# Performance work log

Hardware: AMD Instinct MI355X
Metric: run time of the kernel (lower is better)

Reference implementation:

```python
import jax, jax.numpy as jnp
import numpy as np

N_NODES = 50000
N_EDGES = 800000
IN_CH = 128
HID = 256


def gcn_layer(x, src, dst, W, b, n_nodes):
    # x: [N, F_in] -> h: [N, F_out]
    h = x @ W
    # add self loops (PyG GCNConv default)
    loop = jnp.arange(n_nodes, dtype=src.dtype)
    src_f = jnp.concatenate([src, loop])
    dst_f = jnp.concatenate([dst, loop])
    # symmetric normalization: deg^{-1/2}[src] * deg^{-1/2}[dst]
    deg = jax.ops.segment_sum(jnp.ones_like(dst_f, dtype=h.dtype), dst_f, num_segments=n_nodes)
    dinv = jnp.where(deg > 0, jax.lax.rsqrt(deg), 0.0)
    norm = dinv[src_f] * dinv[dst_f]  # [E+N]
    msg = h[src_f] * norm[:, None]    # [E+N, F_out] gather
    out = jax.ops.segment_sum(msg, dst_f, num_segments=n_nodes)  # scatter-add
    return out + b


def setup_inputs() -> dict:
    key = jax.random.key(0)
    k1, k2, k3, k4 = jax.random.split(key, 4)
    x = jax.random.normal(k1, (N_NODES, IN_CH), dtype=jnp.float32)
    edge_index = jax.random.randint(k2, (2, N_EDGES), 0, N_NODES, dtype=jnp.int64)
    W1 = jax.random.normal(k3, (IN_CH, HID), dtype=jnp.float32) * (1.0 / np.sqrt(IN_CH))
    b1 = jnp.zeros((HID,), dtype=jnp.float32)
    W2 = jax.random.normal(k4, (HID, HID), dtype=jnp.float32) * (1.0 / np.sqrt(HID))
    b2 = jnp.zeros((HID,), dtype=jnp.float32)
    return {"x": x, "edge_index": edge_index, "W1": W1, "b1": b1, "W2": W2, "b2": b2}


def reference(x, edge_index, W1, b1, W2, b2):
    src, dst = edge_index[0], edge_index[1]
    h = gcn_layer(x, src, dst, W1, b1, N_NODES)
    h = jax.nn.relu(h)
    # dropout in eval mode (training=False) is identity
    out = gcn_layer(h, src, dst, W2, b2, N_NODES)
    return out
```

## Files before the change

kernel.cpp:

```cpp
#include <hip/hip_runtime.h>

constexpr int N = 50000;
constexpr int E = 800000;
constexpr int NPAD = 50048;
constexpr int NB = (N + 255) / 256;

typedef _Float16 half8 __attribute__((ext_vector_type(8)));
typedef _Float16 half4v __attribute__((ext_vector_type(4)));
typedef float float4v __attribute__((ext_vector_type(4)));

__global__ __launch_bounds__(256) void deg_kernel(const int* __restrict__ dst,
                                                  int* __restrict__ degI) {
    int e = blockIdx.x * 256 + threadIdx.x;
    if (e < E) atomicAdd(&degI[dst[e]], 1);
}

__global__ __launch_bounds__(256) void dinv_kernel(const int* __restrict__ degI,
                                                   float* __restrict__ dinv) {
    int v = blockIdx.x * 256 + threadIdx.x;
    if (v < N) dinv[v] = rsqrtf((float)degI[v] + 1.0f);
}

__global__ __launch_bounds__(256) void scan1_kernel(const int* __restrict__ degI,
                                                    int* __restrict__ incl,
                                                    int* __restrict__ blockSums) {
    __shared__ int s[256];
    int t = threadIdx.x;
    int i = blockIdx.x * 256 + t;
    int d = (i < N) ? degI[i] : 0;
    s[t] = d;
    __syncthreads();
    for (int off = 1; off < 256; off <<= 1) {
        int v = s[t];
        int u = (t >= off) ? s[t - off] : 0;
        __syncthreads();
        s[t] = v + u;
        __syncthreads();
    }
    if (i < N) incl[i] = s[t];
    if (t == 255) blockSums[blockIdx.x] = s[255];
}

__global__ __launch_bounds__(256) void scan2_kernel(int* __restrict__ blockSums) {
    __shared__ int s[256];
    int t = threadIdx.x;
    int v = (t < NB) ? blockSums[t] : 0;
    s[t] = v;
    __syncthreads();
    for (int off = 1; off < 256; off <<= 1) {
        int a = s[t];
        int u = (t >= off) ? s[t - off] : 0;
        __syncthreads();
        s[t] = a + u;
        __syncthreads();
    }
    if (t < NB) blockSums[t] = s[t] - v;
}

__global__ __launch_bounds__(256) void scan3_kernel(const int* __restrict__ degI,
                                                    const int* __restrict__ incl,
                                                    const int* __restrict__ blockSums,
                                                    int* __restrict__ rowptr,
                                                    int* __restrict__ cursor) {
    int i = blockIdx.x * 256 + threadIdx.x;
    if (i < N) {
        int e = blockSums[blockIdx.x] + incl[i] - degI[i];
        rowptr[i] = e;
        cursor[i] = e;
    }
    if (i == 0) rowptr[N] = E;
}

__global__ __launch_bounds__(256) void fill_kernel(const int* __restrict__ src,
                                                   const int* __restrict__ dst,
                                                   int* __restrict__ cursor,
                                                   int* __restrict__ eidx) {
    int e = blockIdx.x * 256 + threadIdx.x;
    if (e >= E) return;
    int d = dst[e];
    int pos = atomicAdd(&cursor[d], 1);
    eidx[pos] = src[e];
}

template <int K>
__global__ __launch_bounds__(256) void wt_kernel(const float* __restrict__ W,
                                                 _Float16* __restrict__ Wt) {
    int idx = blockIdx.x * 256 + threadIdx.x;
    int k = idx & (K - 1);
    int n = idx >> (K == 128 ? 7 : 8);
    Wt[idx] = (_Float16)W[(size_t)k * 256 + n];
}

__global__ __launch_bounds__(256) void prescale_kernel(const float4* __restrict__ x,
                                                       const float* __restrict__ dinv,
                                                       half4v* __restrict__ px) {
    int idx = blockIdx.x * 256 + threadIdx.x;
    if (idx >= N * 32) return;
    float dv = dinv[idx >> 5];
    float4 t = x[idx];
    half4v o;
    o[0] = (_Float16)(t.x * dv);
    o[1] = (_Float16)(t.y * dv);
    o[2] = (_Float16)(t.z * dv);
    o[3] = (_Float16)(t.w * dv);
    px[idx] = o;
}

template <int C4>
__global__ __launch_bounds__(256) void aggregate_f16(
    const int* __restrict__ rowptr, const int* __restrict__ eidx,
    const half4v* __restrict__ f, const float* __restrict__ dinv,
    half4v* __restrict__ q) {
    int v = blockIdx.x * (256 / C4) + threadIdx.x / C4;
    if (v >= N) return;
    int lane = threadIdx.x % C4;
    int beg = rowptr[v];
    int end = rowptr[v + 1];

    half4v sv = f[(size_t)v * C4 + lane];
    float a0 = (float)sv[0], a1 = (float)sv[1], a2 = (float)sv[2], a3 = (float)sv[3];

    int i = beg;
    for (; i + 8 <= end; i += 8) {
        int e0 = eidx[i + 0], e1 = eidx[i + 1], e2 = eidx[i + 2], e3 = eidx[i + 3];
        int e4 = eidx[i + 4], e5 = eidx[i + 5], e6 = eidx[i + 6], e7 = eidx[i + 7];
        half4v t0 = f[(size_t)e0 * C4 + lane];
        half4v t1 = f[(size_t)e1 * C4 + lane];
        half4v t2 = f[(size_t)e2 * C4 + lane];
        half4v t3 = f[(size_t)e3 * C4 + lane];
        half4v t4 = f[(size_t)e4 * C4 + lane];
        half4v t5 = f[(size_t)e5 * C4 + lane];
        half4v t6 = f[(size_t)e6 * C4 + lane];
        half4v t7 = f[(size_t)e7 * C4 + lane];
        a0 += ((float)t0[0] + (float)t1[0]) + ((float)t2[0] + (float)t3[0]) +
              ((float)t4[0] + (float)t5[0]) + ((float)t6[0] + (float)t7[0]);
        a1 += ((float)t0[1] + (float)t1[1]) + ((float)t2[1] + (float)t3[1]) +
              ((float)t4[1] + (float)t5[1]) + ((float)t6[1] + (float)t7[1]);
        a2 += ((float)t0[2] + (float)t1[2]) + ((float)t2[2] + (float)t3[2]) +
              ((float)t4[2] + (float)t5[2]) + ((float)t6[2] + (float)t7[2]);
        a3 += ((float)t0[3] + (float)t1[3]) + ((float)t2[3] + (float)t3[3]) +
              ((float)t4[3] + (float)t5[3]) + ((float)t6[3] + (float)t7[3]);
    }
    for (; i + 2 <= end; i += 2) {
        int e0 = eidx[i], e1 = eidx[i + 1];
        half4v t0 = f[(size_t)e0 * C4 + lane];
        half4v t1 = f[(size_t)e1 * C4 + lane];
        a0 += (float)t0[0] + (float)t1[0];
        a1 += (float)t0[1] + (float)t1[1];
        a2 += (float)t0[2] + (float)t1[2];
        a3 += (float)t0[3] + (float)t1[3];
    }
    if (i < end) {
        half4v t0 = f[(size_t)eidx[i] * C4 + lane];
        a0 += (float)t0[0];
        a1 += (float)t0[1];
        a2 += (float)t0[2];
        a3 += (float)t0[3];
    }

    float dv = dinv[v];
    half4v o;
    o[0] = (_Float16)(a0 * dv);
    o[1] = (_Float16)(a1 * dv);
    o[2] = (_Float16)(a2 * dv);
    o[3] = (_Float16)(a3 * dv);
    q[(size_t)v * C4 + lane] = o;
}

template <int K, bool FUSE1>
__global__ __launch_bounds__(256) void gemm_mfma(
    const _Float16* __restrict__ A, const _Float16* __restrict__ Wt,
    const float* __restrict__ bias, const float* __restrict__ dinv,
    void* __restrict__ outp) {
    constexpr int LSTR = K + 8;
    __shared__ _Float16 Bs[64 * LSTR];

    const int tid = threadIdx.x;
    const int wave = tid >> 6;
    const int lane = tid & 63;
    const int m = lane & 15;
    const int quad = lane >> 4;
    const int rbase = blockIdx.x * 64 + wave * 16;
    const int row = rbase + m;

    half8 af[K / 32];
    {
        const half8* Arow = (const half8*)(A + (size_t)row * K);
#pragma unroll
        for (int i = 0; i < K / 32; ++i) af[i] = Arow[i * 4 + quad];
    }

    for (int cc = 0; cc < 4; ++cc) {
        const int colbase = cc * 64;
        if (cc) __syncthreads();
        {
            int col = tid >> 2;
            int sub = tid & 3;
            const half8* srcb = (const half8*)(Wt + (size_t)(colbase + col) * K);
            half8* dstb = (half8*)&Bs[col * LSTR];
#pragma unroll
            for (int u = 0; u < K / 32; ++u) dstb[sub + u * 4] = srcb[sub + u * 4];
        }
        __syncthreads();

        float4v acc[4] = {};
#pragma unroll
        for (int k0 = 0; k0 < K; k0 += 32) {
            half8 a = af[k0 >> 5];
#pragma unroll
            for (int c = 0; c < 4; ++c) {
                half8 b = *(const half8*)&Bs[(c * 16 + m) * LSTR + k0 + quad * 8];
                acc[c] = __builtin_amdgcn_mfma_f32_16x16x32_f16(a, b, acc[c], 0, 0, 0);
            }
        }

#pragma unroll
        for (int c = 0; c < 4; ++c) {
            int col = colbase + c * 16 + m;
            float bcol = bias[col];
#pragma unroll
            for (int r = 0; r < 4; ++r) {
                int orow = rbase + quad * 4 + r;
                if (orow < N) {
                    float val = acc[c][r] + bcol;
                    if (FUSE1) {
                        val = fmaxf(val, 0.f) * dinv[orow];
                        ((_Float16*)outp)[(size_t)orow * 256 + col] = (_Float16)val;
                    } else {
                        ((float*)outp)[(size_t)orow * 256 + col] = val;
                    }
                }
            }
        }
    }
}

extern "C" void kernel_launch(void* const* d_in, const int* in_sizes, int n_in,
                              void* d_out, int out_size, void* d_ws, size_t ws_size,
                              hipStream_t stream) {
    const float* x  = (const float*)d_in[0];
    const int* edge = (const int*)d_in[1];
    const int* src  = edge;
    const int* dst  = edge + E;
    const float* W1 = (const float*)d_in[2];
    const float* b1 = (const float*)d_in[3];
    const float* W2 = (const float*)d_in[4];
    const float* b2 = (const float*)d_in[5];
    float* out = (float*)d_out;

    _Float16* bufA = (_Float16*)d_ws;
    _Float16* bufB = bufA + (size_t)NPAD * 256;
    float* dinv    = (float*)(bufB + (size_t)NPAD * 256);
    int* degI      = (int*)(dinv + N);
    int* rowptr    = degI + N;
    int* cursor    = rowptr + (N + 1);
    int* eidx      = cursor + N;
    _Float16* W1t  = (_Float16*)(eidx + E);
    _Float16* W2t  = W1t + 256 * 128;
    int* blockSums = (int*)(W2t + 256 * 256);

    hipMemsetAsync(degI, 0, N * sizeof(int), stream);
    deg_kernel<<<(E + 255) / 256, 256, 0, stream>>>(dst, degI);
    dinv_kernel<<<(N + 255) / 256, 256, 0, stream>>>(degI, dinv);
    scan1_kernel<<<NB, 256, 0, stream>>>(degI, cursor, blockSums);
    scan2_kernel<<<1, 256, 0, stream>>>(blockSums);
    scan3_kernel<<<NB, 256, 0, stream>>>(degI, cursor, blockSums, rowptr, cursor);
    fill_kernel<<<(E + 255) / 256, 256, 0, stream>>>(src, dst, cursor, eidx);

    wt_kernel<128><<<(256 * 128) / 256, 256, 0, stream>>>(W1, W1t);
    wt_kernel<256><<<(256 * 256) / 256, 256, 0, stream>>>(W2, W2t);

    prescale_kernel<<<(N * 32 + 255) / 256, 256, 0, stream>>>(
        (const float4*)x, dinv, (half4v*)bufA);
    aggregate_f16<32><<<(N + 7) / 8, 256, 0, stream>>>(
        rowptr, eidx, (const half4v*)bufA, dinv, (half4v*)bufB);
    gemm_mfma<128, true><<<NPAD / 64, 256, 0, stream>>>(
        bufB, W1t, b1, dinv, bufA);

    aggregate_f16<64><<<(N + 3) / 4, 256, 0, stream>>>(
        rowptr, eidx, (const half4v*)bufA, dinv, (half4v*)bufB);
    gemm_mfma<256, false><<<NPAD / 64, 256, 0, stream>>>(
        bufB, W2t, b2, dinv, out);
}
```

Baseline: 315.8 us.

## Split SpMM aggregation into feature-column chunks mapped across XCDs for L2 locality

Replaces the per-node aggregation kernel with a chunked version. Each block handles 32 nodes times 8 lanes (32 features), and the low 3 bits of blockIdx choose a feature chunk and node segment. With round-robin block dispatch across the 8 XCDs, each XCD's L2 should only see one column slice of the gathered feature matrix, which raises cache hit rates for the random neighbour gathers. In exchange, neighbour indices are re-read once per chunk, and the inner loop unroll drops from 8 to 4.

New measurement: 353.4 us. 11.9% more time.

```diff
diff --git a/kernel.cpp b/kernel.cpp
--- a/kernel.cpp
+++ b/kernel.cpp
@@ -106,56 +106,48 @@
     px[idx] = o;
 }
 
-template <int C4>
-__global__ __launch_bounds__(256) void aggregate_f16(
+template <int T>
+__global__ __launch_bounds__(256) void aggregate_chunked(
     const int* __restrict__ rowptr, const int* __restrict__ eidx,
     const half4v* __restrict__ f, const float* __restrict__ dinv,
     half4v* __restrict__ q) {
-    int v = blockIdx.x * (256 / C4) + threadIdx.x / C4;
-    if (v >= N) return;
-    int lane = threadIdx.x % C4;
-    int beg = rowptr[v];
-    int end = rowptr[v + 1];
-
-    half4v sv = f[(size_t)v * C4 + lane];
-    float a0 = (float)sv[0], a1 = (float)sv[1], a2 = (float)sv[2], a3 = (float)sv[3];
-
-    int i = beg;
-    for (; i + 8 <= end; i += 8) {
+    constexpr int NCHUNK = T / 32;
+    constexpr int NSEG = 8 / NCHUNK;
+    constexpr int SEGN = N / NSEG;
+    constexpr int RS = T / 4;
+
+    const int slot = blockIdx.x & 7;
+    const int chunk = slot & (NCHUNK - 1);
+    const int seg = slot / NCHUNK;
+    const int sub = threadIdx.x >> 3;
+    const int cl = threadIdx.x & 7;
+    const int v = seg * SEGN + (blockIdx.x >> 3) * 32 + sub;
+    if (v >= seg * SEGN + SEGN) return;
+
+    const int coff = chunk * 8 + cl;
+
+    half4v s = f[(size_t)v * RS + coff];
+    float a0 = (float)s[0], a1 = (float)s[1], a2 = (float)s[2], a3 = (float)s[3];
+
+    int i = rowptr[v];
+    const int end = rowptr[v + 1];
+    for (; i + 4 <= end; i += 4) {
         int e0 = eidx[i + 0], e1 = eidx[i + 1], e2 = eidx[i + 2], e3 = eidx[i + 3];
-        int e4 = eidx[i + 4], e5 = eidx[i + 5], e6 = eidx[i + 6], e7 = eidx[i + 7];
-        half4v t0 = f[(size_t)e0 * C4 + lane];
-        half4v t1 = f[(size_t)e1 * C4 + lane];
-        half4v t2 = f[(size_t)e2 * C4 + lane];
-        half4v t3 = f[(size_t)e3 * C4 + lane];
-        half4v t4 = f[(size_t)e4 * C4 + lane];
-        half4v t5 = f[(size_t)e5 * C4 + lane];
-        half4v t6 = f[(size_t)e6 * C4 + lane];
-        half4v t7 = f[(size_t)e7 * C4 + lane];
-        a0 += ((float)t0[0] + (float)t1[0]) + ((float)t2[0] + (float)t3[0]) +
-              ((float)t4[0] + (float)t5[0]) + ((float)t6[0] + (float)t7[0]);
-        a1 += ((float)t0[1] + (float)t1[1]) + ((float)t2[1] + (float)t3[1]) +
-              ((float)t4[1] + (float)t5[1]) + ((float)t6[1] + (float)t7[1]);
-        a2 += ((float)t0[2] + (float)t1[2]) + ((float)t2[2] + (float)t3[2]) +
-              ((float)t4[2] + (float)t5[2]) + ((float)t6[2] + (float)t7[2]);
-        a3 += ((float)t0[3] + (float)t1[3]) + ((float)t2[3] + (float)t3[3]) +
-              ((float)t4[3] + (float)t5[3]) + ((float)t6[3] + (float)t7[3]);
-    }
-    for (; i + 2 <= end; i += 2) {
-        int e0 = eidx[i], e1 = eidx[i + 1];
-        half4v t0 = f[(size_t)e0 * C4 + lane];
-        half4v t1 = f[(size_t)e1 * C4 + lane];
-        a0 += (float)t0[0] + (float)t1[0];
-        a1 += (float)t0[1] + (float)t1[1];
-        a2 += (float)t0[2] + (float)t1[2];
-        a3 += (float)t0[3] + (float)t1[3];
-    }
-    if (i < end) {
-        half4v t0 = f[(size_t)eidx[i] * C4 + lane];
-        a0 += (float)t0[0];
-        a1 += (float)t0[1];
-        a2 += (float)t0[2];
-        a3 += (float)t0[3];
+        half4v t0 = f[(size_t)e0 * RS + coff];
+        half4v t1 = f[(size_t)e1 * RS + coff];
+        half4v t2 = f[(size_t)e2 * RS + coff];
+        half4v t3 = f[(size_t)e3 * RS + coff];
+        a0 += ((float)t0[0] + (float)t1[0]) + ((float)t2[0] + (float)t3[0]);
+        a1 += ((float)t0[1] + (float)t1[1]) + ((float)t2[1] + (float)t3[1]);
+        a2 += ((float)t0[2] + (float)t1[2]) + ((float)t2[2] + (float)t3[2]);
+        a3 += ((float)t0[3] + (float)t1[3]) + ((float)t2[3] + (float)t3[3]);
+    }
+    for (; i < end; ++i) {
+        half4v t = f[(size_t)eidx[i] * RS + coff];
+        a0 += (float)t[0];
+        a1 += (float)t[1];
+        a2 += (float)t[2];
+        a3 += (float)t[3];
     }
 
     float dv = dinv[v];
@@ -164,7 +156,7 @@
     o[1] = (_Float16)(a1 * dv);
     o[2] = (_Float16)(a2 * dv);
     o[3] = (_Float16)(a3 * dv);
-    q[(size_t)v * C4 + lane] = o;
+    q[(size_t)v * RS + coff] = o;
 }
 
 template <int K, bool FUSE1>
@@ -272,12 +264,12 @@
 
     prescale_kernel<<<(N * 32 + 255) / 256, 256, 0, stream>>>(
         (const float4*)x, dinv, (half4v*)bufA);
-    aggregate_f16<32><<<(N + 7) / 8, 256, 0, stream>>>(
+    aggregate_chunked<128><<<8 * ((N / 2 + 31) / 32), 256, 0, stream>>>(
         rowptr, eidx, (const half4v*)bufA, dinv, (half4v*)bufB);
     gemm_mfma<128, true><<<NPAD / 64, 256, 0, stream>>>(
         bufB, W1t, b1, dinv, bufA);
 
-    aggregate_f16<64><<<(N + 3) / 4, 256, 0, stream>>>(
+    aggregate_chunked<256><<<8 * ((N + 31) / 32), 256, 0, stream>>>(
         rowptr, eidx, (const half4v*)bufA, dinv, (half4v*)bufB);
     gemm_mfma<256, false><<<NPAD / 64, 256, 0, stream>>>(
         bufB, W2t, b2, dinv, out);
```

## Merge preprocessing kernels and compute two row tiles per wave in GEMM

Applied to the files above, without the earlier changes.

Several small launches are merged. The degree count and both weight transposes now share one kernel, the dinv computation moves into scan1, and the x prescale moves into scan3 as a grid-stride loop. The MFMA GEMM now gives each wave two 16-row A tiles, so each B fragment loaded from LDS feeds twice as many MFMAs and the grid shrinks to 128 rows per block. This cuts launch overhead and LDS/B-load traffic per output. The cost is that the prescale runs on only NB blocks, which may underuse bandwidth, and the GEMM has fewer blocks and higher register pressure.

Result: slower. 330.2 us (+4.6%).

```diff
diff --git a/kernel.cpp b/kernel.cpp
--- a/kernel.cpp
+++ b/kernel.cpp
@@ -4,30 +4,48 @@
 constexpr int E = 800000;
 constexpr int NPAD = 50048;
 constexpr int NB = (N + 255) / 256;
+constexpr int DEG_BLKS = (E + 255) / 256;
+constexpr int WT_BLKS = (256 * 128 + 256 * 256) / 256;
 
 typedef _Float16 half8 __attribute__((ext_vector_type(8)));
 typedef _Float16 half4v __attribute__((ext_vector_type(4)));
 typedef float float4v __attribute__((ext_vector_type(4)));
 
-__global__ __launch_bounds__(256) void deg_kernel(const int* __restrict__ dst,
-                                                  int* __restrict__ degI) {
-    int e = blockIdx.x * 256 + threadIdx.x;
-    if (e < E) atomicAdd(&degI[dst[e]], 1);
-}
-
-__global__ __launch_bounds__(256) void dinv_kernel(const int* __restrict__ degI,
-                                                   float* __restrict__ dinv) {
-    int v = blockIdx.x * 256 + threadIdx.x;
-    if (v < N) dinv[v] = rsqrtf((float)degI[v] + 1.0f);
+__global__ __launch_bounds__(256) void deg_wt_kernel(const int* __restrict__ dst,
+                                                     int* __restrict__ degI,
+                                                     const float* __restrict__ W1,
+                                                     const float* __restrict__ W2,
+                                                     _Float16* __restrict__ W1t,
+                                                     _Float16* __restrict__ W2t) {
+    int bid = blockIdx.x;
+    int tid = threadIdx.x;
+    if (bid < DEG_BLKS) {
+        int e = bid * 256 + tid;
+        if (e < E) atomicAdd(&degI[dst[e]], 1);
+    } else {
+        int idx = (bid - DEG_BLKS) * 256 + tid;
+        if (idx < 256 * 128) {
+            int k = idx & 127;
+            int n = idx >> 7;
+            W1t[idx] = (_Float16)W1[(size_t)k * 256 + n];
+        } else {
+            int j = idx - 256 * 128;
+            int k = j & 255;
+            int n = j >> 8;
+            W2t[j] = (_Float16)W2[(size_t)k * 256 + n];
+        }
+    }
 }
 
 __global__ __launch_bounds__(256) void scan1_kernel(const int* __restrict__ degI,
                                                     int* __restrict__ incl,
-                                                    int* __restrict__ blockSums) {
+                                                    int* __restrict__ blockSums,
+                                                    float* __restrict__ dinv) {
     __shared__ int s[256];
     int t = threadIdx.x;
     int i = blockIdx.x * 256 + t;
     int d = (i < N) ? degI[i] : 0;
+    if (i < N) dinv[i] = rsqrtf((float)d + 1.0f);
     s[t] = d;
     __syncthreads();
     for (int off = 1; off < 256; off <<= 1) {
@@ -61,14 +79,30 @@
                                                     const int* __restrict__ incl,
                                                     const int* __restrict__ blockSums,
                                                     int* __restrict__ rowptr,
-                                                    int* __restrict__ cursor) {
-    int i = blockIdx.x * 256 + threadIdx.x;
+                                                    int* __restrict__ cursor,
+                                                    const float* __restrict__ dinv,
+                                                    const float4* __restrict__ x,
+                                                    half4v* __restrict__ px) {
+    int t = threadIdx.x;
+    int bid = blockIdx.x;
+    int i = bid * 256 + t;
     if (i < N) {
-        int e = blockSums[blockIdx.x] + incl[i] - degI[i];
+        int e = blockSums[bid] + incl[i] - degI[i];
         rowptr[i] = e;
         cursor[i] = e;
     }
     if (i == 0) rowptr[N] = E;
+
+    for (int idx = bid * 256 + t; idx < N * 32; idx += NB * 256) {
+        float dv = dinv[idx >> 5];
+        float4 tt = x[idx];
+        half4v o;
+        o[0] = (_Float16)(tt.x * dv);
+        o[1] = (_Float16)(tt.y * dv);
+        o[2] = (_Float16)(tt.z * dv);
+        o[3] = (_Float16)(tt.w * dv);
+        px[idx] = o;
+    }
 }
 
 __global__ __launch_bounds__(256) void fill_kernel(const int* __restrict__ src,
@@ -80,30 +114,6 @@
     int d = dst[e];
     int pos = atomicAdd(&cursor[d], 1);
     eidx[pos] = src[e];
-}
-
-template <int K>
-__global__ __launch_bounds__(256) void wt_kernel(const float* __restrict__ W,
-                                                 _Float16* __restrict__ Wt) {
-    int idx = blockIdx.x * 256 + threadIdx.x;
-    int k = idx & (K - 1);
-    int n = idx >> (K == 128 ? 7 : 8);
-    Wt[idx] = (_Float16)W[(size_t)k * 256 + n];
-}
-
-__global__ __launch_bounds__(256) void prescale_kernel(const float4* __restrict__ x,
-                                                       const float* __restrict__ dinv,
-                                                       half4v* __restrict__ px) {
-    int idx = blockIdx.x * 256 + threadIdx.x;
-    if (idx >= N * 32) return;
-    float dv = dinv[idx >> 5];
-    float4 t = x[idx];
-    half4v o;
-    o[0] = (_Float16)(t.x * dv);
-    o[1] = (_Float16)(t.y * dv);
-    o[2] = (_Float16)(t.z * dv);
-    o[3] = (_Float16)(t.w * dv);
-    px[idx] = o;
 }
 
 template <int C4>
@@ -180,14 +190,14 @@
     const int lane = tid & 63;
     const int m = lane & 15;
     const int quad = lane >> 4;
-    const int rbase = blockIdx.x * 64 + wave * 16;
-    const int row = rbase + m;
-
-    half8 af[K / 32];
-    {
-        const half8* Arow = (const half8*)(A + (size_t)row * K);
-#pragma unroll
-        for (int i = 0; i < K / 32; ++i) af[i] = Arow[i * 4 + quad];
+    const int rbase = blockIdx.x * 128 + wave * 32;
+
+    half8 af[2][K / 32];
+#pragma unroll
+    for (int rr = 0; rr < 2; ++rr) {
+        const half8* Arow = (const half8*)(A + (size_t)(rbase + rr * 16 + m) * K);
+#pragma unroll
+        for (int i = 0; i < K / 32; ++i) af[rr][i] = Arow[i * 4 + quad];
     }
 
     for (int cc = 0; cc < 4; ++cc) {
@@ -203,14 +213,16 @@
         }
         __syncthreads();
 
-        float4v acc[4] = {};
+        float4v acc[2][4] = {};
 #pragma unroll
         for (int k0 = 0; k0 < K; k0 += 32) {
-            half8 a = af[k0 >> 5];
+            half8 a0 = af[0][k0 >> 5];
+            half8 a1 = af[1][k0 >> 5];
 #pragma unroll
             for (int c = 0; c < 4; ++c) {
                 half8 b = *(const half8*)&Bs[(c * 16 + m) * LSTR + k0 + quad * 8];
-                acc[c] = __builtin_amdgcn_mfma_f32_16x16x32_f16(a, b, acc[c], 0, 0, 0);
+                acc[0][c] = __builtin_amdgcn_mfma_f32_16x16x32_f16(a0, b, acc[0][c], 0, 0, 0);
+                acc[1][c] = __builtin_amdgcn_mfma_f32_16x16x32_f16(a1, b, acc[1][c], 0, 0, 0);
             }
         }
 
@@ -219,15 +231,18 @@
             int col = colbase + c * 16 + m;
             float bcol = bias[col];
 #pragma unroll
-            for (int r = 0; r < 4; ++r) {
-                int orow = rbase + quad * 4 + r;
-                if (orow < N) {
-                    float val = acc[c][r] + bcol;
-                    if (FUSE1) {
-                        val = fmaxf(val, 0.f) * dinv[orow];
-                        ((_Float16*)outp)[(size_t)orow * 256 + col] = (_Float16)val;
-                    } else {
-                        ((float*)outp)[(size_t)orow * 256 + col] = val;
+            for (int rr = 0; rr < 2; ++rr) {
+#pragma unroll
+                for (int r = 0; r < 4; ++r) {
+                    int orow = rbase + rr * 16 + quad * 4 + r;
+                    if (orow < N) {
+                        float val = acc[rr][c][r] + bcol;
+                        if (FUSE1) {
+                            val = fmaxf(val, 0.f) * dinv[orow];
+                            ((_Float16*)outp)[(size_t)orow * 256 + col] = (_Float16)val;
+                        } else {
+                            ((float*)outp)[(size_t)orow * 256 + col] = val;
+                        }
                     }
                 }
             }
@@ -260,25 +275,21 @@
     int* blockSums = (int*)(W2t + 256 * 256);
 
     hipMemsetAsync(degI, 0, N * sizeof(int), stream);
-    deg_kernel<<<(E + 255) / 256, 256, 0, stream>>>(dst, degI);
-    dinv_kernel<<<(N + 255) / 256, 256, 0, stream>>>(degI, dinv);
-    scan1_kernel<<<NB, 256, 0, stream>>>(degI, cursor, blockSums);
+    deg_wt_kernel<<<DEG_BLKS + WT_BLKS, 256, 0, stream>>>(
+        dst, degI, W1, W2, W1t, W2t);
+    scan1_kernel<<<NB, 256, 0, stream>>>(degI, cursor, blockSums, dinv);
     scan2_kernel<<<1, 256, 0, stream>>>(blockSums);
-    scan3_kernel<<<NB, 256, 0, stream>>>(degI, cursor, blockSums, rowptr, cursor);
-    fill_kernel<<<(E + 255) / 256, 256, 0, stream>>>(src, dst, cursor, eidx);
-
-    wt_kernel<128><<<(256 * 128) / 256, 256, 0, stream>>>(W1, W1t);
-    wt_kernel<256><<<(256 * 256) / 256, 256, 0, stream>>>(W2, W2t);
-
-    prescale_kernel<<<(N * 32 + 255) / 256, 256, 0, stream>>>(
-        (const float4*)x, dinv, (half4v*)bufA);
+    scan3_kernel<<<NB, 256, 0, stream>>>(degI, cursor, blockSums, rowptr, cursor,
+                                         dinv, (const float4*)x, (half4v*)bufA);
+    fill_kernel<<<DEG_BLKS, 256, 0, stream>>>(src, dst, cursor, eidx);
+
     aggregate_f16<32><<<(N + 7) / 8, 256, 0, stream>>>(
         rowptr, eidx, (const half4v*)bufA, dinv, (half4v*)bufB);
-    gemm_mfma<128, true><<<NPAD / 64, 256, 0, stream>>>(
+    gemm_mfma<128, true><<<NPAD / 128, 256, 0, stream>>>(
         bufB, W1t, b1, dinv, bufA);
 
     aggregate_f16<64><<<(N + 3) / 4, 256, 0, stream>>>(
         rowptr, eidx, (const half4v*)bufA, dinv, (half4v*)bufB);
-    gemm_mfma<256, false><<<NPAD / 64, 256, 0, stream>>>(
+    gemm_mfma<256, false><<<NPAD / 128, 256, 0, stream>>>(
         bufB, W2t, b2, dinv, out);
 }
```
